# Performance work log

Measured on AMD Instinct MI355X. Metric: run time of the kernel, lower is better.

Reference implementation:

```python
import jax, jax.numpy as jnp
import numpy as np
from jax import lax

N_NODES = 100000
N_EDGES = 6400000


def setup_inputs() -> dict:
    key = jax.random.key(0)
    k1, k2, k3, k4 = jax.random.split(key, 4)
    values = jax.random.uniform(k1, (N_NODES,), dtype=jnp.float32)
    edge_weights = jax.random.normal(k2, (N_EDGES,), dtype=jnp.float32)
    neighbor_idx = jax.random.randint(k3, (N_EDGES,), 0, N_NODES, dtype=jnp.int64 if jax.config.jax_enable_x64 else jnp.int32)
    segment_ids = jnp.sort(jax.random.randint(k4, (N_EDGES,), 0, N_NODES, dtype=jnp.int64 if jax.config.jax_enable_x64 else jnp.int32))
    return {
        "values": values,
        "edge_weights": edge_weights,
        "neighbor_idx": neighbor_idx,
        "segment_ids": segment_ids,
        "n_times": 3,
    }


def reference(values, edge_weights, neighbor_idx, segment_ids, n_times):
    # One forward_once: for each node i, new[i] = sigmoid(sum_{e: dst(e)=i} w_e * values[src(e)])
    # (per-node Linear(num_links, 1, bias=False) + Sigmoid, flattened over the ragged edge list)
    n_nodes = values.shape[0]

    def step(v, _):
        msgs = edge_weights * v[neighbor_idx]                      # [n_edges]
        agg = jax.ops.segment_sum(msgs, segment_ids, num_segments=n_nodes)
        return jax.nn.sigmoid(agg), None

    out, _ = lax.scan(step, values, None, length=int(n_times))
    return out
```

## Files before the change

kernel.cpp:

```cpp
#include <hip/hip_runtime.h>
#include <hip/hip_bf16.h>

#define N_NODES_DEFAULT 100000

__global__ void ppgcn_offsets(const int* __restrict__ seg, int n_edges, int n_nodes,
                              int* __restrict__ offs) {
    int i = blockIdx.x * blockDim.x + threadIdx.x;
    if (i > n_nodes) return;
    int lo = 0, hi = n_edges;
    while (lo < hi) {
        int mid = (lo + hi) >> 1;
        if (seg[mid] < i) lo = mid + 1; else hi = mid;
    }
    offs[i] = lo;
}

__global__ __launch_bounds__(256) void ppgcn_step(const float* __restrict__ vin,
                                                  const float* __restrict__ w,
                                                  const int* __restrict__ idx,
                                                  const int* __restrict__ offs,
                                                  float* __restrict__ vout,
                                                  int n_nodes) {
    int wave = (int)((blockIdx.x * (unsigned)blockDim.x + threadIdx.x) >> 6);
    int lane = threadIdx.x & 63;
    if (wave >= n_nodes) return;
    int start = offs[wave];
    int end   = offs[wave + 1];
    float sum = 0.0f;
    for (int e = start + lane; e < end; e += 64) {
        sum += w[e] * vin[idx[e]];
    }
    #pragma unroll
    for (int off = 32; off > 0; off >>= 1)
        sum += __shfl_down(sum, off, 64);
    if (lane == 0)
        vout[wave] = 1.0f / (1.0f + expf(-sum));
}

extern "C" void kernel_launch(void* const* d_in, const int* in_sizes, int n_in,
                              void* d_out, int out_size, void* d_ws, size_t ws_size,
                              hipStream_t stream) {
    const float* values       = (const float*)d_in[0];
    const float* edge_weights = (const float*)d_in[1];
    const int*   neighbor_idx = (const int*)d_in[2];
    const int*   segment_ids  = (const int*)d_in[3];

    const int n_nodes = in_sizes[0];
    const int n_edges = in_sizes[1];

    char* ws = (char*)d_ws;
    int*   offs = (int*)ws;
    size_t offs_bytes = ((size_t)(n_nodes + 1) * sizeof(int) + 255) & ~(size_t)255;
    float* bufA = (float*)(ws + offs_bytes);
    size_t buf_bytes = ((size_t)n_nodes * sizeof(float) + 255) & ~(size_t)255;
    float* bufB = (float*)(ws + offs_bytes + buf_bytes);
    float* out  = (float*)d_out;

    {
        int threads = 256;
        int blocks = (n_nodes + 1 + threads - 1) / threads;
        ppgcn_offsets<<<blocks, threads, 0, stream>>>(segment_ids, n_edges, n_nodes, offs);
    }

    int threads = 256;
    int waves_per_block = threads / 64;
    int blocks = (n_nodes + waves_per_block - 1) / waves_per_block;

    ppgcn_step<<<blocks, threads, 0, stream>>>(values, edge_weights, neighbor_idx, offs, bufA, n_nodes);
    ppgcn_step<<<blocks, threads, 0, stream>>>(bufA,   edge_weights, neighbor_idx, offs, bufB, n_nodes);
    ppgcn_step<<<blocks, threads, 0, stream>>>(bufB,   edge_weights, neighbor_idx, offs, out,  n_nodes);
}
```

Baseline: 117.7 us.

## Build CSR offsets by boundary scan and use 16-lane groups per node

Replaces the per-node binary search over segment ids with a streaming pass where each thread reads eight sorted ids (vectorized) and writes offsets at segment boundaries. The step kernel now assigns 16 lanes per node instead of a full 64-lane wave, matching the average of about 64 edges per node. It also unrolls the first six strided iterations with predication to expose more independent gathers, and uses the fast exp intrinsic. Nodes with many edges get less parallelism, and the scan assumes the segment ids are sorted.

After: 114.5 us. 1.03x faster.

```diff
diff --git a/kernel.cpp b/kernel.cpp
--- a/kernel.cpp
+++ b/kernel.cpp
@@ -1,18 +1,43 @@
 #include <hip/hip_runtime.h>
 #include <hip/hip_bf16.h>
 
-#define N_NODES_DEFAULT 100000
+#define EPT 8
 
-__global__ void ppgcn_offsets(const int* __restrict__ seg, int n_edges, int n_nodes,
-                              int* __restrict__ offs) {
-    int i = blockIdx.x * blockDim.x + threadIdx.x;
-    if (i > n_nodes) return;
-    int lo = 0, hi = n_edges;
-    while (lo < hi) {
-        int mid = (lo + hi) >> 1;
-        if (seg[mid] < i) lo = mid + 1; else hi = mid;
+__global__ __launch_bounds__(256) void ppgcn_offsets_scan(const int* __restrict__ seg,
+                                                          int n_edges, int n_nodes,
+                                                          int* __restrict__ offs) {
+    int t = blockIdx.x * blockDim.x + threadIdx.x;
+    long long e0 = (long long)t * EPT;
+    if (e0 >= n_edges) return;
+
+    int prev = (e0 == 0) ? -1 : seg[e0 - 1];
+
+    int vals[EPT];
+    if (e0 + EPT <= n_edges && ((e0 & 3) == 0)) {
+        const int4* p4 = reinterpret_cast<const int4*>(seg + e0);
+        int4 a = p4[0];
+        int4 b = p4[1];
+        vals[0]=a.x; vals[1]=a.y; vals[2]=a.z; vals[3]=a.w;
+        vals[4]=b.x; vals[5]=b.y; vals[6]=b.z; vals[7]=b.w;
+    } else {
+        #pragma unroll
+        for (int j = 0; j < EPT; ++j)
+            vals[j] = (e0 + j < n_edges) ? seg[e0 + j] : 0;
     }
-    offs[i] = lo;
+
+    #pragma unroll
+    for (int j = 0; j < EPT; ++j) {
+        long long e = e0 + j;
+        if (e >= n_edges) break;
+        int cur = vals[j];
+        for (int k = prev + 1; k <= cur; ++k)
+            offs[k] = (int)e;
+        prev = cur;
+    }
+    if (e0 + EPT >= n_edges) {
+        for (int k = prev + 1; k <= n_nodes; ++k)
+            offs[k] = n_edges;
+    }
 }
 
 __global__ __launch_bounds__(256) void ppgcn_step(const float* __restrict__ vin,
@@ -21,20 +46,34 @@
                                                   const int* __restrict__ offs,
                                                   float* __restrict__ vout,
                                                   int n_nodes) {
-    int wave = (int)((blockIdx.x * (unsigned)blockDim.x + threadIdx.x) >> 6);
-    int lane = threadIdx.x & 63;
-    if (wave >= n_nodes) return;
-    int start = offs[wave];
-    int end   = offs[wave + 1];
+    int gid = (int)((blockIdx.x * 256u + threadIdx.x) >> 4);
+    int sl  = threadIdx.x & 15;
+    if (gid >= n_nodes) return;
+
+    int start = offs[gid];
+    int end   = offs[gid + 1];
+
     float sum = 0.0f;
-    for (int e = start + lane; e < end; e += 64) {
-        sum += w[e] * vin[idx[e]];
+    int e = start + sl;
+
+    #pragma unroll
+    for (int j = 0; j < 6; ++j) {
+        int ee = e + j * 16;
+        bool p = ee < end;
+        int   ii = p ? idx[ee] : 0;
+        float wv = p ? w[ee]  : 0.0f;
+        sum += wv * vin[ii];
     }
-    #pragma unroll
-    for (int off = 32; off > 0; off >>= 1)
-        sum += __shfl_down(sum, off, 64);
-    if (lane == 0)
-        vout[wave] = 1.0f / (1.0f + expf(-sum));
+    for (int ee = e + 96; ee < end; ee += 16)
+        sum += w[ee] * vin[idx[ee]];
+
+    sum += __shfl_xor(sum, 8, 64);
+    sum += __shfl_xor(sum, 4, 64);
+    sum += __shfl_xor(sum, 2, 64);
+    sum += __shfl_xor(sum, 1, 64);
+
+    if (sl == 0)
+        vout[gid] = 1.0f / (1.0f + __expf(-sum));
 }
 
 extern "C" void kernel_launch(void* const* d_in, const int* in_sizes, int n_in,
@@ -58,13 +97,14 @@
 
     {
         int threads = 256;
-        int blocks = (n_nodes + 1 + threads - 1) / threads;
-        ppgcn_offsets<<<blocks, threads, 0, stream>>>(segment_ids, n_edges, n_nodes, offs);
+        int total_threads = (n_edges + EPT - 1) / EPT;
+        int blocks = (total_threads + threads - 1) / threads;
+        ppgcn_offsets_scan<<<blocks, threads, 0, stream>>>(segment_ids, n_edges, n_nodes, offs);
     }
 
     int threads = 256;
-    int waves_per_block = threads / 64;
-    int blocks = (n_nodes + waves_per_block - 1) / waves_per_block;
+    int nodes_per_block = threads / 16;
+    int blocks = (n_nodes + nodes_per_block - 1) / nodes_per_block;
 
     ppgcn_step<<<blocks, threads, 0, stream>>>(values, edge_weights, neighbor_idx, offs, bufA, n_nodes);
     ppgcn_step<<<blocks, threads, 0, stream>>>(bufA,   edge_weights, neighbor_idx, offs, bufB, n_nodes);
```

## Switch from wave-per-node CSR reduction to edge-parallel segmented atomics

Applied to the files above, without the earlier changes.

Drops the binary-search offsets kernel and the one-wave-per-node reduction. Each thread now processes 16 consecutive edges with vectorized loads, does a run-length segmented sum over the sorted segment ids, and flushes partial sums with atomics. A separate small kernel applies the sigmoid and zeroes the accumulator. The aim is to raise memory-level parallelism and balance the work. The cost is reading the segment ids on every step, atomic traffic, and summation order that is no longer deterministic.

Result: slower. 160.9 us (+36.6%).

```diff
diff --git a/kernel.cpp b/kernel.cpp
--- a/kernel.cpp
+++ b/kernel.cpp
@@ -1,40 +1,68 @@
 #include <hip/hip_runtime.h>
 #include <hip/hip_bf16.h>
 
-#define N_NODES_DEFAULT 100000
+#define EPT 16
 
-__global__ void ppgcn_offsets(const int* __restrict__ seg, int n_edges, int n_nodes,
-                              int* __restrict__ offs) {
-    int i = blockIdx.x * blockDim.x + threadIdx.x;
-    if (i > n_nodes) return;
-    int lo = 0, hi = n_edges;
-    while (lo < hi) {
-        int mid = (lo + hi) >> 1;
-        if (seg[mid] < i) lo = mid + 1; else hi = mid;
+__global__ __launch_bounds__(256) void ppgcn_edges(const float* __restrict__ vin,
+                                                   const float* __restrict__ w,
+                                                   const int* __restrict__ idx,
+                                                   const int* __restrict__ seg,
+                                                   float* __restrict__ acc,
+                                                   int n_edges) {
+    long long t = (long long)blockIdx.x * blockDim.x + threadIdx.x;
+    long long e0 = t * EPT;
+    if (e0 >= n_edges) return;
+
+    if (e0 + EPT <= n_edges) {
+        const int4*   ip = reinterpret_cast<const int4*>(idx + e0);
+        const float4* wp = reinterpret_cast<const float4*>(w + e0);
+        const int4*   sp = reinterpret_cast<const int4*>(seg + e0);
+        int4 i4[4]; float4 w4[4]; int4 s4[4];
+        #pragma unroll
+        for (int q = 0; q < 4; ++q) i4[q] = ip[q];
+        #pragma unroll
+        for (int q = 0; q < 4; ++q) w4[q] = wp[q];
+        #pragma unroll
+        for (int q = 0; q < 4; ++q) s4[q] = sp[q];
+
+        int ii[EPT]; float ww[EPT]; int ss[EPT];
+        #pragma unroll
+        for (int q = 0; q < 4; ++q) {
+            ii[4*q+0] = i4[q].x; ii[4*q+1] = i4[q].y; ii[4*q+2] = i4[q].z; ii[4*q+3] = i4[q].w;
+            ww[4*q+0] = w4[q].x; ww[4*q+1] = w4[q].y; ww[4*q+2] = w4[q].z; ww[4*q+3] = w4[q].w;
+            ss[4*q+0] = s4[q].x; ss[4*q+1] = s4[q].y; ss[4*q+2] = s4[q].z; ss[4*q+3] = s4[q].w;
+        }
+
+        float g[EPT];
+        #pragma unroll
+        for (int j = 0; j < EPT; ++j) g[j] = vin[ii[j]];
+
+        float run = 0.0f; int cur = ss[0];
+        #pragma unroll
+        for (int j = 0; j < EPT; ++j) {
+            if (ss[j] != cur) { unsafeAtomicAdd(&acc[cur], run); run = 0.0f; cur = ss[j]; }
+            run = fmaf(ww[j], g[j], run);
+        }
+        unsafeAtomicAdd(&acc[cur], run);
+    } else {
+        float run = 0.0f; int cur = seg[e0];
+        for (long long e = e0; e < n_edges; ++e) {
+            int s = seg[e];
+            if (s != cur) { unsafeAtomicAdd(&acc[cur], run); run = 0.0f; cur = s; }
+            run += w[e] * vin[idx[e]];
+        }
+        unsafeAtomicAdd(&acc[cur], run);
     }
-    offs[i] = lo;
 }
 
-__global__ __launch_bounds__(256) void ppgcn_step(const float* __restrict__ vin,
-                                                  const float* __restrict__ w,
-                                                  const int* __restrict__ idx,
-                                                  const int* __restrict__ offs,
-                                                  float* __restrict__ vout,
-                                                  int n_nodes) {
-    int wave = (int)((blockIdx.x * (unsigned)blockDim.x + threadIdx.x) >> 6);
-    int lane = threadIdx.x & 63;
-    if (wave >= n_nodes) return;
-    int start = offs[wave];
-    int end   = offs[wave + 1];
-    float sum = 0.0f;
-    for (int e = start + lane; e < end; e += 64) {
-        sum += w[e] * vin[idx[e]];
-    }
-    #pragma unroll
-    for (int off = 32; off > 0; off >>= 1)
-        sum += __shfl_down(sum, off, 64);
-    if (lane == 0)
-        vout[wave] = 1.0f / (1.0f + expf(-sum));
+__global__ __launch_bounds__(256) void ppgcn_sigmoid_reset(float* __restrict__ acc,
+                                                           float* __restrict__ vout,
+                                                           int n_nodes) {
+    int i = blockIdx.x * blockDim.x + threadIdx.x;
+    if (i >= n_nodes) return;
+    float a = acc[i];
+    vout[i] = 1.0f / (1.0f + expf(-a));
+    acc[i] = 0.0f;
 }
 
 extern "C" void kernel_launch(void* const* d_in, const int* in_sizes, int n_in,
@@ -49,24 +77,24 @@
     const int n_edges = in_sizes[1];
 
     char* ws = (char*)d_ws;
-    int*   offs = (int*)ws;
-    size_t offs_bytes = ((size_t)(n_nodes + 1) * sizeof(int) + 255) & ~(size_t)255;
-    float* bufA = (float*)(ws + offs_bytes);
-    size_t buf_bytes = ((size_t)n_nodes * sizeof(float) + 255) & ~(size_t)255;
-    float* bufB = (float*)(ws + offs_bytes + buf_bytes);
+    size_t abytes = ((size_t)n_nodes * sizeof(float) + 255) & ~(size_t)255;
+    float* acc  = (float*)ws;
+    float* bufA = (float*)(ws + abytes);
+    float* bufB = (float*)(ws + 2 * abytes);
     float* out  = (float*)d_out;
 
-    {
-        int threads = 256;
-        int blocks = (n_nodes + 1 + threads - 1) / threads;
-        ppgcn_offsets<<<blocks, threads, 0, stream>>>(segment_ids, n_edges, n_nodes, offs);
-    }
+    hipMemsetAsync(acc, 0, (size_t)n_nodes * sizeof(float), stream);
 
-    int threads = 256;
-    int waves_per_block = threads / 64;
-    int blocks = (n_nodes + waves_per_block - 1) / waves_per_block;
+    int ethreads = (n_edges + EPT - 1) / EPT;
+    int eblocks  = (ethreads + 255) / 256;
+    int nblocks  = (n_nodes + 255) / 256;
 
-    ppgcn_step<<<blocks, threads, 0, stream>>>(values, edge_weights, neighbor_idx, offs, bufA, n_nodes);
-    ppgcn_step<<<blocks, threads, 0, stream>>>(bufA,   edge_weights, neighbor_idx, offs, bufB, n_nodes);
-    ppgcn_step<<<blocks, threads, 0, stream>>>(bufB,   edge_weights, neighbor_idx, offs, out,  n_nodes);
+    ppgcn_edges<<<eblocks, 256, 0, stream>>>(values, edge_weights, neighbor_idx, segment_ids, acc, n_edges);
+    ppgcn_sigmoid_reset<<<nblocks, 256, 0, stream>>>(acc, bufA, n_nodes);
+
+    ppgcn_edges<<<eblocks, 256, 0, stream>>>(bufA, edge_weights, neighbor_idx, segment_ids, acc, n_edges);
+    ppgcn_sigmoid_reset<<<nblocks, 256, 0, stream>>>(acc, bufB, n_nodes);
+
+    ppgcn_edges<<<eblocks, 256, 0, stream>>>(bufB, edge_weights, neighbor_idx, segment_ids, acc, n_edges);
+    ppgcn_sigmoid_reset<<<nblocks, 256, 0, stream>>>(acc, out, n_nodes);
 }
```
